# Optimization experiments

Measured on AMD Instinct MI355X. Metric: run time of the kernel, lower is better.

Reference implementation:

```python
import jax, jax.numpy as jnp
import numpy as np

N_NODES = 100000
N_EDGES = 3200000
N_FEAT = 500
HIDDEN = 128
N_CLASSES = 64
K_LAYERS = 10
ALPHA = 0.1


def setup_inputs() -> dict:
    key = jax.random.key(0)
    k_x, k_e, k_w1, k_b1, k_w2, k_b2 = jax.random.split(key, 6)
    x = jax.random.normal(k_x, (N_NODES, N_FEAT), dtype=jnp.float32)
    edge_index = jax.random.randint(k_e, (2, N_EDGES), 0, N_NODES, dtype=jnp.int64)
    # Linear layers (torch nn.Linear default init ~ U(-1/sqrt(fan_in), 1/sqrt(fan_in)))
    s1 = 1.0 / np.sqrt(N_FEAT)
    s2 = 1.0 / np.sqrt(HIDDEN)
    W1 = jax.random.uniform(k_w1, (N_FEAT, HIDDEN), jnp.float32, -s1, s1)
    b1 = jax.random.uniform(k_b1, (HIDDEN,), jnp.float32, -s1, s1)
    W2 = jax.random.uniform(k_w2, (HIDDEN, N_CLASSES), jnp.float32, -s2, s2)
    b2 = jax.random.uniform(k_b2, (N_CLASSES,), jnp.float32, -s2, s2)
    return {"x": x, "edge_index": edge_index, "W1": W1, "b1": b1, "W2": W2, "b2": b2}


def reference(x, edge_index, W1, b1, W2, b2):
    n = x.shape[0]
    # MLP: Linear -> ReLU -> Linear
    h = jnp.maximum(x @ W1 + b1, 0.0) @ W2 + b2  # [N, C]

    # GCN symmetric normalization with self-loops (PyG APPNP / gcn_norm)
    loops = jnp.arange(n, dtype=edge_index.dtype)
    src = jnp.concatenate([edge_index[0], loops])
    dst = jnp.concatenate([edge_index[1], loops])
    deg = jax.ops.segment_sum(jnp.ones_like(dst, dtype=h.dtype), dst, num_segments=n)
    dinv = jnp.where(deg > 0, jax.lax.rsqrt(deg), 0.0)
    norm = dinv[src] * dinv[dst]  # [E+N]

    h0 = h

    def step(z, _):
        msgs = z[src] * norm[:, None]                       # gather over edges
        agg = jax.ops.segment_sum(msgs, dst, num_segments=n)  # scatter-add
        z_new = (1.0 - ALPHA) * agg + ALPHA * h0
        return z_new, None

    z, _ = jax.lax.scan(step, h0, None, length=K_LAYERS)
    return jax.nn.softmax(z, axis=1)
```

## Files before the change

### kernel.cpp

```cpp
#include <hip/hip_runtime.h>
#include <hip/hip_bf16.h>
#include <hip/hip_fp16.h>

#define N_NODES   100000
#define N_EDGES   3200000
#define N_FEAT    500
#define HIDDEN    128
#define N_CLASSES 64
#define K_LAYERS  10
#define NBUCK     98

typedef __attribute__((ext_vector_type(4))) float f32x4;
typedef __attribute__((ext_vector_type(8))) _Float16 f16x8;

__device__ inline float2 h2f2(unsigned u) {
  __half2 h = *(__half2*)&u;
  return make_float2(__low2float(h), __high2float(h));
}
__device__ inline unsigned f2h2(float a, float b) {
  __half2 h = __floats2half2_rn(a, b);
  return *(unsigned*)&h;
}


__global__ __launch_bounds__(256) void bucket_count_k(const int* __restrict__ dst,
                                                      int* __restrict__ bucket_cnt) {
  __shared__ int h[128];
  int t = threadIdx.x;
  if (t < 128) h[t] = 0;
  __syncthreads();
  for (int e = blockIdx.x * 256 + t; e < N_EDGES; e += gridDim.x * 256)
    atomicAdd(&h[dst[e] >> 10], 1);
  __syncthreads();
  if (t < 128 && h[t]) atomicAdd(&bucket_cnt[t], h[t]);
}

__global__ __launch_bounds__(128) void bucket_scan_k(const int* __restrict__ bucket_cnt,
                                                     int* __restrict__ bucket_base,
                                                     int* __restrict__ bcur,
                                                     int* __restrict__ offs) {
  __shared__ int sm[128];
  int t = threadIdx.x;
  int c = bucket_cnt[t];
  sm[t] = c;
  __syncthreads();
  for (int d = 1; d < 128; d <<= 1) {
    int v = (t >= d) ? sm[t - d] : 0;
    __syncthreads();
    sm[t] += v;
    __syncthreads();
  }
  int ex = sm[t] - c;
  bucket_base[t] = ex;
  bcur[t] = ex;
  if (t == 127) bucket_base[128] = ex + c;
  if (t == 0) offs[N_NODES] = N_EDGES;
}

#define BIN_CHUNK 12800
__global__ __launch_bounds__(256) void bin_scatter_k(const int* __restrict__ src,
                                                     const int* __restrict__ dst,
                                                     int* __restrict__ bcur,
                                                     int* __restrict__ binned) {
  __shared__ int h[128];
  __shared__ int hbase[128];
  int t = threadIdx.x;
  int e0 = blockIdx.x * BIN_CHUNK;
  int e1 = min(e0 + BIN_CHUNK, N_EDGES);
  if (t < 128) h[t] = 0;
  __syncthreads();
  for (int e = e0 + t; e < e1; e += 256) atomicAdd(&h[dst[e] >> 10], 1);
  __syncthreads();
  if (t < 128) {
    int c = h[t];
    hbase[t] = c ? atomicAdd(&bcur[t], c) : 0;
  }
  __syncthreads();
  if (t < 128) h[t] = 0;
  __syncthreads();
  for (int e = e0 + t; e < e1; e += 256) {
    int d = dst[e];
    int b = d >> 10;
    int pos = hbase[b] + atomicAdd(&h[b], 1);
    binned[pos] = (src[e] & 0x1FFFF) | ((d & 1023) << 17);
  }
}

__global__ __launch_bounds__(256) void bucket_fill_k(const int* __restrict__ binned,
                                                     const int* __restrict__ bucket_base,
                                                     int* __restrict__ offs,
                                                     float* __restrict__ dinv,
                                                     int* __restrict__ csr4) {
  __shared__ int cnt[1024];
  __shared__ int tsum[256];
  int b = blockIdx.x;
  int base = bucket_base[b];
  int nE = bucket_base[b + 1] - base;
  int node0 = b << 10;
  int nN = min(1024, N_NODES - node0);
  int t = threadIdx.x;
  #pragma unroll
  for (int i = 0; i < 4; ++i) cnt[t + i * 256] = 0;
  __syncthreads();
  for (int i = t; i < nE; i += 256) atomicAdd(&cnt[binned[base + i] >> 17], 1);
  __syncthreads();
  int c0 = cnt[4 * t], c1 = cnt[4 * t + 1], c2 = cnt[4 * t + 2], c3 = cnt[4 * t + 3];
  int s = c0 + c1 + c2 + c3;
  tsum[t] = s;
  __syncthreads();
  for (int d = 1; d < 256; d <<= 1) {
    int v = (t >= d) ? tsum[t - d] : 0;
    __syncthreads();
    tsum[t] += v;
    __syncthreads();
  }
  int run = tsum[t] - s;
  int p0 = run, p1 = run + c0, p2 = p1 + c1, p3 = p2 + c2;
  if (4 * t + 0 < nN) { offs[node0 + 4 * t + 0] = base + p0; dinv[node0 + 4 * t + 0] = rsqrtf(c0 + 1.f); }
  if (4 * t + 1 < nN) { offs[node0 + 4 * t + 1] = base + p1; dinv[node0 + 4 * t + 1] = rsqrtf(c1 + 1.f); }
  if (4 * t + 2 < nN) { offs[node0 + 4 * t + 2] = base + p2; dinv[node0 + 4 * t + 2] = rsqrtf(c2 + 1.f); }
  if (4 * t + 3 < nN) { offs[node0 + 4 * t + 3] = base + p3; dinv[node0 + 4 * t + 3] = rsqrtf(c3 + 1.f); }
  __syncthreads();
  cnt[4 * t] = p0; cnt[4 * t + 1] = p1; cnt[4 * t + 2] = p2; cnt[4 * t + 3] = p3;
  __syncthreads();
  for (int i = t; i < nE; i += 256) {
    int rec = binned[base + i];
    int p = base + atomicAdd(&cnt[rec >> 17], 1);
    csr4[p] = rec & 0x1FFFF;
  }
}

__global__ void prep_wsw_k(const float* __restrict__ W, ushort* __restrict__ Bsw,
                           int KTOT, int BN, int KPAD) {
  int g = blockIdx.x * 256 + threadIdx.x;
  if (g >= BN * KPAD) return;
  int chunk = BN * 64;
  int s = g / chunk;
  int r = g - s * chunk;
  int c = r >> 6;
  int q = r & 63;
  int X = (q >> 3) ^ (c & 7);
  int e = q & 7;
  int k = s * 64 + X * 8 + e;
  float v = (k < KTOT) ? W[(size_t)k * BN + c] : 0.f;
  _Float16 hv = (_Float16)v;
  Bsw[g] = *(ushort*)&hv;
}

template<int BN, int KTOT, int KPAD, bool RELU, bool A16, bool C16>
__device__ __forceinline__ void gemm_core(const void* Ain, const ushort* Bsw,
                                          const float* bias, void* Cout, int M) {
  constexpr int BK = 64;
  constexpr int NS = KPAD / BK;
  constexpr int NF = BN / 16;
  constexpr int CHUNK = BN * BK;
  constexpr int NL = CHUNK * 2 / (16 * 256);
  __shared__ __align__(16) ushort Bl[2][CHUNK];

  int tid = threadIdx.x;
  int lane = tid & 63, w = tid >> 6;
  int lrow = lane & 15, lg = lane >> 4;
  int row0 = blockIdx.x * 128 + w * 32;

  const float* A32 = (const float*)Ain;
  const ushort* Ah = (const ushort*)Ain;

  f32x4 acc[2][NF];
  #pragma unroll
  for (int m = 0; m < 2; ++m)
    #pragma unroll
    for (int n = 0; n < NF; ++n) acc[m][n] = (f32x4){0.f, 0.f, 0.f, 0.f};

  #define STAGE(s, buf)                                                   \
    {                                                                     \
      const ushort* gp = Bsw + (size_t)(s) * CHUNK;                       \
      _Pragma("unroll")                                                   \
      for (int i = 0; i < NL; ++i) {                                      \
        int o = (tid + i * 256) * 8;                                      \
        __builtin_amdgcn_global_load_lds(gp + o, &Bl[buf][o], 16, 0, 0);  \
      }                                                                   \
    }

  STAGE(0, 0);
  asm volatile("s_waitcnt vmcnt(0)" ::: "memory");
  __syncthreads();

  #pragma unroll 1
  for (int s = 0; s < NS; ++s) {
    int cur = s & 1;
    if (s + 1 < NS) STAGE(s + 1, cur ^ 1);
    int kc = s * BK;
    #pragma unroll
    for (int ks = 0; ks < 2; ++ks) {
      f16x8 af[2];
      #pragma unroll
      for (int m = 0; m < 2; ++m) {
        int r = row0 + m * 16 + lrow;
        int rc = r < M ? r : M - 1;
        int k0 = kc + ks * 32 + lg * 8;
        if (A16) {
          af[m] = *(const f16x8*)(Ah + (size_t)rc * KPAD + k0);
        } else {
          const float* ap = A32 + (size_t)rc * KTOT + k0;
          f16x8 h;
          if (k0 + 7 < KTOT) {
            float4 f0 = *(const float4*)ap;
            float4 f1 = *(const float4*)(ap + 4);
            h[0] = (_Float16)f0.x; h[1] = (_Float16)f0.y;
            h[2] = (_Float16)f0.z; h[3] = (_Float16)f0.w;
            h[4] = (_Float16)f1.x; h[5] = (_Float16)f1.y;
            h[6] = (_Float16)f1.z; h[7] = (_Float16)f1.w;
          } else {
            #pragma unroll
            for (int e = 0; e < 8; ++e)
              h[e] = (_Float16)((k0 + e < KTOT) ? ap[e] : 0.f);
          }
          af[m] = h;
        }
      }
      #pragma unroll
      for (int n = 0; n < NF; ++n) {
        int c = n * 16 + lrow;
        int ad = c * 64 + ((((ks << 2) + lg) ^ (c & 7)) << 3);
        f16x8 bf = *(const f16x8*)(&Bl[cur][ad]);
        #pragma unroll
        for (int m = 0; m < 2; ++m)
          acc[m][n] = __builtin_amdgcn_mfma_f32_16x16x32_f16(af[m], bf, acc[m][n], 0, 0, 0);
      }
    }
    asm volatile("s_waitcnt vmcnt(0)" ::: "memory");
    __syncthreads();
  }
  #undef STAGE

  #pragma unroll
  for (int m = 0; m < 2; ++m)
    #pragma unroll
    for (int n = 0; n < NF; ++n) {
      int c = n * 16 + lrow;
      float bb = bias[c];
      #pragma unroll
      for (int r4 = 0; r4 < 4; ++r4) {
        int grow = row0 + m * 16 + lg * 4 + r4;
        if (grow < M) {
          float v = acc[m][n][r4] + bb;
          if (RELU) v = fmaxf(v, 0.f);
          if (C16) {
            _Float16 hv = (_Float16)v;
            ((ushort*)Cout)[(size_t)grow * BN + c] = *(ushort*)&hv;
          } else {
            ((float*)Cout)[(size_t)grow * BN + c] = v;
          }
        }
      }
    }
}

__global__ __launch_bounds__(256, 2) void gemm1_k(const float* __restrict__ A,
                                                  const ushort* __restrict__ Bsw,
                                                  const float* __restrict__ bias,
                                                  ushort* __restrict__ C, int M) {
  gemm_core<128, 500, 512, true, false, true>(A, Bsw, bias, C, M);
}
__global__ __launch_bounds__(256, 2) void gemm2_k(const ushort* __restrict__ A,
                                                  const ushort* __restrict__ Bsw,
                                                  const float* __restrict__ bias,
                                                  float* __restrict__ C, int M) {
  gemm_core<64, 128, 128, false, true, false>(A, Bsw, bias, C, M);
}

__global__ __launch_bounds__(256) void conv_y0_k(const float* __restrict__ h0,
                                                 const float* __restrict__ dinv,
                                                 uint2* __restrict__ y16) {
  int i = blockIdx.x * 256 + threadIdx.x;
  if (i >= N_NODES * 16) return;
  int node = i >> 4;
  float dv = dinv[node];
  float4 h4 = ((const float4*)h0)[i];
  y16[i] = make_uint2(f2h2(dv * h4.x, dv * h4.y), f2h2(dv * h4.z, dv * h4.w));
}

template<bool OUT32>
__global__ __launch_bounds__(256) void prop_k(const uint2* __restrict__ yin,
                                              void* __restrict__ out,
                                              const float* __restrict__ h0,
                                              const float* __restrict__ dinv,
                                              const int* __restrict__ offs,
                                              const int* __restrict__ csr4) {
  int lane = threadIdx.x & 63;
  int wid = threadIdx.x >> 6;
  int node = (blockIdx.x << 2) + wid;
  if (node >= N_NODES) return;
  int grp = lane >> 4;
  int lc = lane & 15;

  float4 acc = make_float4(0.f, 0.f, 0.f, 0.f);
  int beg = offs[node], end = offs[node + 1];
  for (int e = beg; e < end; e += 64) {
    int s = (e + lane < end) ? csr4[e + lane] : N_NODES;
    int cnt = min(64, end - e);
    for (int j = 0; j < cnt; j += 32) {
      int sr[8];
      uint2 g[8];
      #pragma unroll
      for (int q = 0; q < 8; ++q) sr[q] = __shfl(s, j + 4 * q + grp);
      #pragma unroll
      for (int q = 0; q < 8; ++q) g[q] = yin[(size_t)sr[q] * 16 + lc];
      #pragma unroll
      for (int q = 0; q < 8; ++q) {
        float2 a = h2f2(g[q].x), b = h2f2(g[q].y);
        acc.x += a.x; acc.y += a.y; acc.z += b.x; acc.w += b.y;
      }
    }
  }
  #pragma unroll
  for (int off = 16; off <= 32; off <<= 1) {
    acc.x += __shfl_xor(acc.x, off);
    acc.y += __shfl_xor(acc.y, off);
    acc.z += __shfl_xor(acc.z, off);
    acc.w += __shfl_xor(acc.w, off);
  }
  if (grp == 0) {
    uint2 gs = yin[(size_t)node * 16 + lc];
    float2 a = h2f2(gs.x), b = h2f2(gs.y);
    acc.x += a.x; acc.y += a.y; acc.z += b.x; acc.w += b.y;
    float dv = dinv[node];
    float4 h4 = ((const float4*)h0)[(size_t)node * 16 + lc];
    float4 z;
    z.x = 0.9f * dv * acc.x + 0.1f * h4.x;
    z.y = 0.9f * dv * acc.y + 0.1f * h4.y;
    z.z = 0.9f * dv * acc.z + 0.1f * h4.z;
    z.w = 0.9f * dv * acc.w + 0.1f * h4.w;
    if (OUT32) {
      ((float4*)out)[(size_t)node * 16 + lc] = z;
    } else {
      ((uint2*)out)[(size_t)node * 16 + lc] =
          make_uint2(f2h2(dv * z.x, dv * z.y), f2h2(dv * z.z, dv * z.w));
    }
  }
}

__global__ __launch_bounds__(256) void softmax_k(const float* __restrict__ z,
                                                 float* __restrict__ out) {
  int lane = threadIdx.x & 63;
  int row = (blockIdx.x * 256 + threadIdx.x) >> 6;
  if (row >= N_NODES) return;
  float v = z[(size_t)row * 64 + lane];
  float m = v;
  #pragma unroll
  for (int o = 32; o > 0; o >>= 1) m = fmaxf(m, __shfl_xor(m, o));
  float ev = __expf(v - m);
  float s = ev;
  #pragma unroll
  for (int o = 32; o > 0; o >>= 1) s += __shfl_xor(s, o);
  out[(size_t)row * 64 + lane] = ev / s;
}

extern "C" void kernel_launch(void* const* d_in, const int* in_sizes, int n_in,
                              void* d_out, int out_size, void* d_ws, size_t ws_size,
                              hipStream_t stream) {
  const float* x  = (const float*)d_in[0];
  const int*   ei = (const int*)d_in[1];
  const float* W1 = (const float*)d_in[2];
  const float* b1 = (const float*)d_in[3];
  const float* W2 = (const float*)d_in[4];
  const float* b2 = (const float*)d_in[5];
  const int* src = ei;
  const int* dst = ei + N_EDGES;

  char* w = (char*)d_ws;
  int*    csr4  = (int*)w;
  ushort* H     = (ushort*)(w + 12800000);
  uint2*  zA16  = (uint2*)(w + 12800000);
  uint2*  zB16  = (uint2*)(w + 25700000);
  float*  zF32  = (float*)(w + 38600000);
  int*    binned = (int*)(w + 38600000);
  float*  dinv  = (float*)(w + 64500000);
  int*    offs  = (int*)(w + 65000000);
  int*    bucket_cnt  = (int*)(w + 66000000);
  int*    bucket_base = (int*)(w + 66002048);
  int*    bcur        = (int*)(w + 66004096);
  ushort* w1sw  = (ushort*)(w + 66500000);
  ushort* w2sw  = (ushort*)(w + 66700000);
  float* h0 = (float*)d_out;

  hipMemsetAsync(bucket_cnt, 0, 128 * 4, stream);

  bucket_count_k<<<512, 256, 0, stream>>>(dst, bucket_cnt);
  bucket_scan_k<<<1, 128, 0, stream>>>(bucket_cnt, bucket_base, bcur, offs);
  bin_scatter_k<<<N_EDGES / BIN_CHUNK, 256, 0, stream>>>(src, dst, bcur, binned);
  bucket_fill_k<<<NBUCK, 256, 0, stream>>>(binned, bucket_base, offs, dinv, csr4);

  prep_wsw_k<<<(128 * 512 + 255) / 256, 256, 0, stream>>>(W1, w1sw, 500, 128, 512);
  prep_wsw_k<<<(64 * 128 + 255) / 256, 256, 0, stream>>>(W2, w2sw, 128, 64, 128);
  gemm1_k<<<(N_NODES + 127) / 128, 256, 0, stream>>>(x, w1sw, b1, H, N_NODES);
  gemm2_k<<<(N_NODES + 127) / 128, 256, 0, stream>>>(H, w2sw, b2, h0, N_NODES);

  hipMemsetAsync((char*)zA16 + (size_t)N_NODES * 128, 0, 128, stream);
  hipMemsetAsync((char*)zB16 + (size_t)N_NODES * 128, 0, 128, stream);

  conv_y0_k<<<(N_NODES * 16 + 255) / 256, 256, 0, stream>>>(h0, dinv, zA16);

  const uint2* zi = zA16;
  uint2* zo = zB16;
  for (int it = 0; it < K_LAYERS - 1; ++it) {
    prop_k<false><<<(N_NODES + 3) / 4, 256, 0, stream>>>(zi, (void*)zo, h0, dinv, offs, csr4);
    zi = zo;
    zo = (zo == zA16) ? zB16 : zA16;
  }
  prop_k<true><<<(N_NODES + 3) / 4, 256, 0, stream>>>(zi, (void*)zF32, h0, dinv, offs, csr4);

  softmax_k<<<(N_NODES * 64) / 256, 256, 0, stream>>>(zF32, (float*)d_out);
}
```

Measured before the change: 993.8 us.

## Split propagation features into four column slabs to shrink gather working set

The 64-class feature matrix is split into four 16-column slabs, each stored contiguously (fp32 for h0, fp16 for the propagated state). Each propagation launch now uses a 2D grid where blockIdx.y selects a slab, so each gathered row is 32 bytes instead of 128. The aim is to make each slab's random-gather working set small enough to stay in cache. In exchange, every edge index is read four times and the number of gather instructions per edge grows. Softmax now runs in place on the output buffer.

```diff
diff --git a/kernel.cpp b/kernel.cpp
--- a/kernel.cpp
+++ b/kernel.cpp
@@ -9,6 +9,8 @@
 #define N_CLASSES 64
 #define K_LAYERS  10
 #define NBUCK     98
+#define SLU       400004
+#define SLF4      400004
 
 typedef __attribute__((ext_vector_type(4))) float f32x4;
 typedef __attribute__((ext_vector_type(8))) _Float16 f16x8;
@@ -147,7 +149,7 @@
   Bsw[g] = *(ushort*)&hv;
 }
 
-template<int BN, int KTOT, int KPAD, bool RELU, bool A16, bool C16>
+template<int BN, int KTOT, int KPAD, bool RELU, bool A16, int CMODE>
 __device__ __forceinline__ void gemm_core(const void* Ain, const ushort* Bsw,
                                           const float* bias, void* Cout, int M) {
   constexpr int BK = 64;
@@ -245,11 +247,13 @@
         if (grow < M) {
           float v = acc[m][n][r4] + bb;
           if (RELU) v = fmaxf(v, 0.f);
-          if (C16) {
+          if (CMODE == 0) {
+            ((float*)Cout)[(size_t)grow * BN + c] = v;
+          } else if (CMODE == 1) {
             _Float16 hv = (_Float16)v;
             ((ushort*)Cout)[(size_t)grow * BN + c] = *(ushort*)&hv;
           } else {
-            ((float*)Cout)[(size_t)grow * BN + c] = v;
+            ((float*)Cout)[(size_t)(c >> 4) * (4 * SLF4) + (size_t)grow * 16 + (c & 15)] = v;
           }
         }
       }
@@ -260,88 +264,96 @@
                                                   const ushort* __restrict__ Bsw,
                                                   const float* __restrict__ bias,
                                                   ushort* __restrict__ C, int M) {
-  gemm_core<128, 500, 512, true, false, true>(A, Bsw, bias, C, M);
+  gemm_core<128, 500, 512, true, false, 1>(A, Bsw, bias, C, M);
 }
 __global__ __launch_bounds__(256, 2) void gemm2_k(const ushort* __restrict__ A,
                                                   const ushort* __restrict__ Bsw,
                                                   const float* __restrict__ bias,
                                                   float* __restrict__ C, int M) {
-  gemm_core<64, 128, 128, false, true, false>(A, Bsw, bias, C, M);
-}
-
-__global__ __launch_bounds__(256) void conv_y0_k(const float* __restrict__ h0,
+  gemm_core<64, 128, 128, false, true, 2>(A, Bsw, bias, C, M);
+}
+
+__global__ void pad_zero_k(uint2* __restrict__ yA, uint2* __restrict__ yB) {
+  int t = threadIdx.x;
+  if (t >= 32) return;
+  uint2* b = (t & 16) ? yB : yA;
+  int p = (t >> 2) & 3, lc = t & 3;
+  b[(size_t)p * SLU + (size_t)N_NODES * 4 + lc] = make_uint2(0, 0);
+}
+
+__global__ __launch_bounds__(256) void conv_y0_k(const float4* __restrict__ h0sl4,
                                                  const float* __restrict__ dinv,
                                                  uint2* __restrict__ y16) {
-  int i = blockIdx.x * 256 + threadIdx.x;
-  if (i >= N_NODES * 16) return;
-  int node = i >> 4;
+  int j = blockIdx.x * 256 + threadIdx.x;
+  if (j >= N_NODES * 4) return;
+  int p = blockIdx.y;
+  int node = j >> 2;
   float dv = dinv[node];
-  float4 h4 = ((const float4*)h0)[i];
-  y16[i] = make_uint2(f2h2(dv * h4.x, dv * h4.y), f2h2(dv * h4.z, dv * h4.w));
+  float4 h4 = h0sl4[(size_t)p * SLF4 + j];
+  y16[(size_t)p * SLU + j] =
+      make_uint2(f2h2(dv * h4.x, dv * h4.y), f2h2(dv * h4.z, dv * h4.w));
 }
 
 template<bool OUT32>
-__global__ __launch_bounds__(256) void prop_k(const uint2* __restrict__ yin,
-                                              void* __restrict__ out,
-                                              const float* __restrict__ h0,
-                                              const float* __restrict__ dinv,
-                                              const int* __restrict__ offs,
-                                              const int* __restrict__ csr4) {
+__global__ __launch_bounds__(256) void prop_s_k(const uint2* __restrict__ yin,
+                                                void* __restrict__ out,
+                                                const float4* __restrict__ h0sl4,
+                                                const float* __restrict__ dinv,
+                                                const int* __restrict__ offs,
+                                                const int* __restrict__ csr4) {
+  int p = blockIdx.y;
   int lane = threadIdx.x & 63;
   int wid = threadIdx.x >> 6;
   int node = (blockIdx.x << 2) + wid;
   if (node >= N_NODES) return;
-  int grp = lane >> 4;
-  int lc = lane & 15;
+  int grp = lane >> 2;
+  int lc = lane & 3;
+  const uint2* ys = yin + (size_t)p * SLU;
 
   float4 acc = make_float4(0.f, 0.f, 0.f, 0.f);
   int beg = offs[node], end = offs[node + 1];
   for (int e = beg; e < end; e += 64) {
     int s = (e + lane < end) ? csr4[e + lane] : N_NODES;
-    int cnt = min(64, end - e);
-    for (int j = 0; j < cnt; j += 32) {
-      int sr[8];
-      uint2 g[8];
-      #pragma unroll
-      for (int q = 0; q < 8; ++q) sr[q] = __shfl(s, j + 4 * q + grp);
-      #pragma unroll
-      for (int q = 0; q < 8; ++q) g[q] = yin[(size_t)sr[q] * 16 + lc];
-      #pragma unroll
-      for (int q = 0; q < 8; ++q) {
-        float2 a = h2f2(g[q].x), b = h2f2(g[q].y);
-        acc.x += a.x; acc.y += a.y; acc.z += b.x; acc.w += b.y;
-      }
+    int sr[4];
+    uint2 g[4];
+    #pragma unroll
+    for (int q = 0; q < 4; ++q) sr[q] = __shfl(s, q * 16 + grp);
+    #pragma unroll
+    for (int q = 0; q < 4; ++q) g[q] = ys[(size_t)sr[q] * 4 + lc];
+    #pragma unroll
+    for (int q = 0; q < 4; ++q) {
+      float2 a = h2f2(g[q].x), b = h2f2(g[q].y);
+      acc.x += a.x; acc.y += a.y; acc.z += b.x; acc.w += b.y;
     }
   }
   #pragma unroll
-  for (int off = 16; off <= 32; off <<= 1) {
+  for (int off = 4; off <= 32; off <<= 1) {
     acc.x += __shfl_xor(acc.x, off);
     acc.y += __shfl_xor(acc.y, off);
     acc.z += __shfl_xor(acc.z, off);
     acc.w += __shfl_xor(acc.w, off);
   }
   if (grp == 0) {
-    uint2 gs = yin[(size_t)node * 16 + lc];
+    uint2 gs = ys[(size_t)node * 4 + lc];
     float2 a = h2f2(gs.x), b = h2f2(gs.y);
     acc.x += a.x; acc.y += a.y; acc.z += b.x; acc.w += b.y;
     float dv = dinv[node];
-    float4 h4 = ((const float4*)h0)[(size_t)node * 16 + lc];
+    float4 h4 = h0sl4[(size_t)p * SLF4 + (size_t)node * 4 + lc];
     float4 z;
     z.x = 0.9f * dv * acc.x + 0.1f * h4.x;
     z.y = 0.9f * dv * acc.y + 0.1f * h4.y;
     z.z = 0.9f * dv * acc.z + 0.1f * h4.z;
     z.w = 0.9f * dv * acc.w + 0.1f * h4.w;
     if (OUT32) {
-      ((float4*)out)[(size_t)node * 16 + lc] = z;
+      ((float4*)out)[(size_t)node * 16 + p * 4 + lc] = z;
     } else {
-      ((uint2*)out)[(size_t)node * 16 + lc] =
+      ((uint2*)out)[(size_t)p * SLU + (size_t)node * 4 + lc] =
           make_uint2(f2h2(dv * z.x, dv * z.y), f2h2(dv * z.z, dv * z.w));
     }
   }
 }
 
-__global__ __launch_bounds__(256) void softmax_k(const float* __restrict__ z,
-                                                 float* __restrict__ out) {
+__global__ __launch_bounds__(256) void softmax_k(const float* z, float* out) {
   int lane = threadIdx.x & 63;
   int row = (blockIdx.x * 256 + threadIdx.x) >> 6;
   if (row >= N_NODES) return;
@@ -371,10 +383,10 @@
   char* w = (char*)d_ws;
   int*    csr4  = (int*)w;
   ushort* H     = (ushort*)(w + 12800000);
-  uint2*  zA16  = (uint2*)(w + 12800000);
-  uint2*  zB16  = (uint2*)(w + 25700000);
-  float*  zF32  = (float*)(w + 38600000);
+  uint2*  yA    = (uint2*)(w + 12800000);
+  uint2*  yB    = (uint2*)(w + 25700000);
   int*    binned = (int*)(w + 38600000);
+  float*  h0sl  = (float*)(w + 38600000);
   float*  dinv  = (float*)(w + 64500000);
   int*    offs  = (int*)(w + 65000000);
   int*    bucket_cnt  = (int*)(w + 66000000);
@@ -382,7 +394,6 @@
   int*    bcur        = (int*)(w + 66004096);
   ushort* w1sw  = (ushort*)(w + 66500000);
   ushort* w2sw  = (ushort*)(w + 66700000);
-  float* h0 = (float*)d_out;
 
   hipMemsetAsync(bucket_cnt, 0, 128 * 4, stream);
 
@@ -394,21 +405,22 @@
   prep_wsw_k<<<(128 * 512 + 255) / 256, 256, 0, stream>>>(W1, w1sw, 500, 128, 512);
   prep_wsw_k<<<(64 * 128 + 255) / 256, 256, 0, stream>>>(W2, w2sw, 128, 64, 128);
   gemm1_k<<<(N_NODES + 127) / 128, 256, 0, stream>>>(x, w1sw, b1, H, N_NODES);
-  gemm2_k<<<(N_NODES + 127) / 128, 256, 0, stream>>>(H, w2sw, b2, h0, N_NODES);
-
-  hipMemsetAsync((char*)zA16 + (size_t)N_NODES * 128, 0, 128, stream);
-  hipMemsetAsync((char*)zB16 + (size_t)N_NODES * 128, 0, 128, stream);
-
-  conv_y0_k<<<(N_NODES * 16 + 255) / 256, 256, 0, stream>>>(h0, dinv, zA16);
-
-  const uint2* zi = zA16;
-  uint2* zo = zB16;
+  gemm2_k<<<(N_NODES + 127) / 128, 256, 0, stream>>>(H, w2sw, b2, h0sl, N_NODES);
+
+  pad_zero_k<<<1, 64, 0, stream>>>(yA, yB);
+  conv_y0_k<<<dim3((N_NODES * 4 + 255) / 256, 4), 256, 0, stream>>>(
+      (const float4*)h0sl, dinv, yA);
+
+  const uint2* zi = yA;
+  uint2* zo = yB;
   for (int it = 0; it < K_LAYERS - 1; ++it) {
-    prop_k<false><<<(N_NODES + 3) / 4, 256, 0, stream>>>(zi, (void*)zo, h0, dinv, offs, csr4);
+    prop_s_k<false><<<dim3(N_NODES / 4, 4), 256, 0, stream>>>(
+        zi, (void*)zo, (const float4*)h0sl, dinv, offs, csr4);
     zi = zo;
-    zo = (zo == zA16) ? zB16 : zA16;
-  }
-  prop_k<true><<<(N_NODES + 3) / 4, 256, 0, stream>>>(zi, (void*)zF32, h0, dinv, offs, csr4);
-
-  softmax_k<<<(N_NODES * 64) / 256, 256, 0, stream>>>(zF32, (float*)d_out);
-}
+    zo = (zo == yA) ? yB : yA;
+  }
+  prop_s_k<true><<<dim3(N_NODES / 4, 4), 256, 0, stream>>>(
+      zi, d_out, (const float4*)h0sl, dinv, offs, csr4);
+
+  softmax_k<<<(N_NODES * 64) / 256, 256, 0, stream>>>((float*)d_out, (float*)d_out);
+}
```

New measurement: 1.479 ms. +48.8%, slower.
